# Kernel optimization log

Hardware: AMD Instinct MI355X
Metric: run time of the kernel (lower is better)

## Reference

```python
import jax, jax.numpy as jnp
import numpy as np
from jax import lax

# ---- config (mirrors cfg.* used by the module) ----
ANCHOR_RATIOS = (0.5, 1.0, 2.0)
ANCHOR_SCALES = (8.0, 16.0, 32.0)
FEATURE_STRIDE = 16
BASE_SIZE = 40  # generate_anchors(40, ...)
BN_EPS = 1e-5
LOG_CLAMP = 1e-30  # torch uses 1e-300, which underflows to 0 in fp32; use fp32-safe tiny


def generate_anchors(base_size=BASE_SIZE, ratios=ANCHOR_RATIOS, scales=ANCHOR_SCALES):
    """py-faster-rcnn style anchor generation, corner format (x1,y1,x2,y2). -> (A,4)"""
    w = h = float(base_size)
    cx = (base_size - 1) * 0.5
    cy = (base_size - 1) * 0.5
    size = w * h
    out = []
    for r in ratios:
        ws = np.round(np.sqrt(size / r))
        hs = np.round(ws * r)
        for s in scales:
            W, H = ws * s, hs * s
            out.append([cx - 0.5 * (W - 1), cy - 0.5 * (H - 1),
                        cx + 0.5 * (W - 1), cy + 0.5 * (H - 1)])
    return np.asarray(out, dtype=np.float32)  # (A,4)


def splash_anchors(fH, fW, n, base_anchors, stride):
    """Shift base anchors over the feature grid. -> (n, fH*fW*A, 4), row-major H,W then A."""
    sx = jnp.arange(fW, dtype=jnp.float32) * stride
    sy = jnp.arange(fH, dtype=jnp.float32) * stride
    SY, SX = jnp.meshgrid(sy, sx, indexing='ij')            # (fH,fW)
    shifts = jnp.stack([SX, SY, SX, SY], axis=-1).reshape(-1, 1, 4)  # (fH*fW,1,4)
    anc = (shifts + jnp.asarray(base_anchors)[None, :, :]).reshape(-1, 4)  # (fH*fW*A,4)
    return jnp.broadcast_to(anc[None], (n, anc.shape[0], 4))


def conv2d(x, w, b, pad):
    y = lax.conv_general_dilated(x, w, (1, 1), [(pad, pad), (pad, pad)],
                                 dimension_numbers=('NCHW', 'OIHW', 'NCHW'))
    return y + b[None, :, None, None]


def batchnorm_train(x, gamma, beta):
    # training-mode BN: per-channel batch stats over (N,H,W), biased variance
    m = jnp.mean(x, axis=(0, 2, 3), keepdims=True)
    v = jnp.mean(jnp.square(x - m), axis=(0, 2, 3), keepdims=True)
    xn = (x - m) * lax.rsqrt(v + BN_EPS)
    return xn * gamma[None, :, None, None] + beta[None, :, None, None]


def mish(x):
    return x * jnp.tanh(jax.nn.softplus(x))


def corner2center(b):
    w = b[..., 2] - b[..., 0]
    h = b[..., 3] - b[..., 1]
    cx = b[..., 0] + 0.5 * w
    cy = b[..., 1] + 0.5 * h
    return jnp.stack([cx, cy, w, h], axis=-1)


def setup_inputs() -> dict:
    key = jax.random.key(0)
    ks = jax.random.split(key, 7)
    C_IN, C_BASE, A = 256, 256, 9
    x = jax.random.normal(ks[0], (8, C_IN, 128, 128), dtype=jnp.float32)
    # kaiming-uniform-ish scaled weights
    def kaiming(k, shape):
        fan_in = shape[1] * shape[2] * shape[3]
        bound = float(np.sqrt(6.0 / fan_in))
        return jax.random.uniform(k, shape, jnp.float32, -bound, bound)
    return {
        "x": x,
        "W_base": kaiming(ks[1], (C_BASE, C_IN, 3, 3)),
        "b_base": jnp.zeros((C_BASE,), jnp.float32),
        "g_base": jnp.ones((C_BASE,), jnp.float32),
        "be_base": jnp.zeros((C_BASE,), jnp.float32),
        "W_cls": kaiming(ks[2], (2 * A, C_BASE, 1, 1)),
        "b_cls": jnp.zeros((2 * A,), jnp.float32),
        "g_cls": jnp.ones((2 * A,), jnp.float32),
        "be_cls": jnp.zeros((2 * A,), jnp.float32),
        "W_reg": kaiming(ks[3], (4 * A, C_BASE, 1, 1)),
        "b_reg": jnp.zeros((4 * A,), jnp.float32),
        "g_reg": jnp.ones((4 * A,), jnp.float32),
        "be_reg": jnp.zeros((4 * A,), jnp.float32),
        "img_size": 2048,
    }


def reference(x, W_base, b_base, g_base, be_base,
              W_cls, b_cls, g_cls, be_cls,
              W_reg, b_reg, g_reg, be_reg, img_size):
    n, c, fH, fW = x.shape
    A = 9
    # BASE_CONV: Conv3x3 -> Mish -> Dropout2d (identity here, deterministic) -> BN
    base = batchnorm_train(mish(conv2d(x, W_base, b_base, 1)), g_base, be_base)

    anchors = splash_anchors(fH, fW, n, generate_anchors(), FEATURE_STRIDE)  # (n,K,4) corners

    rpn_reg = batchnorm_train(conv2d(base, W_reg, b_reg, 0), g_reg, be_reg)
    rpn_reg = jnp.transpose(rpn_reg, (0, 2, 3, 1)).reshape(n, -1, 4)          # (n,K,4)

    rpn_score = batchnorm_train(conv2d(base, W_cls, b_cls, 0), g_cls, be_cls)
    rpn_score = jnp.transpose(rpn_score, (0, 2, 3, 1)).reshape(n, fH, fW, A, 2)
    fg_scores = jax.nn.softmax(rpn_score, axis=4)[..., 1].reshape(n, -1)      # (n,K)

    rpn_reg = rpn_reg + anchors                                               # decoded corners

    # proposal layer: clip proposals to the image, keep all (fixed-shape)
    lim = jnp.float32(img_size)
    rois = jnp.clip(rpn_reg, 0.0, lim)                                        # (n,K,4) corners
    rois = corner2center(rois)                                                # (cx,cy,w,h)

    anc_c = corner2center(anchors)
    tx = (rois[..., 0] - anc_c[..., 0]) / anc_c[..., 2]
    ty = (rois[..., 1] - anc_c[..., 1]) / anc_c[..., 3]
    tw = jnp.log(jnp.maximum(rois[..., 2] / anc_c[..., 2], LOG_CLAMP))
    th = jnp.log(jnp.maximum(rois[..., 3] / anc_c[..., 3], LOG_CLAMP))
    ts = jnp.stack([tx, ty, tw, th], axis=-1)
    return (fg_scores, ts, rois)
```

## Files before the change

### kernel.cpp

```cpp
#include <hip/hip_runtime.h>
#include <stdint.h>

typedef short bf16x8 __attribute__((ext_vector_type(8)));
typedef float f32x4 __attribute__((ext_vector_type(4)));

#define AS1 __attribute__((address_space(1)))
#define AS3 __attribute__((address_space(3)))

static __device__ __forceinline__ void gl16(const void* g, void* l) {
  __builtin_amdgcn_global_load_lds((const AS1 void*)g, (AS3 void*)l, 16, 0, 0);
}

static __device__ __forceinline__ unsigned short f2bf(float f) {
  unsigned u = __float_as_uint(f);
  u = u + 0x7fffu + ((u >> 16) & 1u);
  return (unsigned short)(u >> 16);
}
static __device__ __forceinline__ float bf2f(unsigned short h) {
  return __uint_as_float(((unsigned)h) << 16);
}
static __device__ __forceinline__ float mishf(float x) {
  float sp = fmaxf(x, 0.f) + log1pf(expf(-fabsf(x)));
  float e2 = expf(-2.f * sp);
  float th = (1.f - e2) / (1.f + e2);
  return x * th;
}

#define NIMG 8
#define HH 128
#define WW 128
#define HP 130
#define CIN 256
#define MPIX (NIMG * HH * WW)
#define KTOT 2304
#define FGCNT (MPIX * 9)
#define TSCNT (MPIX * 9 * 4)

__device__ __constant__ float AW[9] = {456.f, 912.f, 1824.f, 320.f, 640.f, 1280.f, 224.f, 448.f, 896.f};
__device__ __constant__ float AH[9] = {224.f, 448.f, 896.f, 320.f, 640.f, 1280.f, 448.f, 896.f, 1792.f};

__global__ __launch_bounds__(256) void k_wt(const float* __restrict__ Wb,
                                            unsigned short* __restrict__ Wt2) {
  int d = blockIdx.x * 256 + threadIdx.x;
  int c = d & 31, oc = (d >> 5) & 255, s = d >> 13;
  int icb = s / 9, khw = s % 9, kh = khw / 3, kw = khw % 3;
  int ic = icb * 32 + c;
  Wt2[d] = f2bf(Wb[((oc * 256 + ic) * 3 + kh) * 3 + kw]);
}

__global__ __launch_bounds__(256) void k_tr(const float* __restrict__ x,
                                            unsigned short* __restrict__ xt2) {
  __shared__ float tile[32][129];
  int b = blockIdx.x;
  int icb = b & 7, h = (b >> 3) & 127, n = b >> 10;
  int t = threadIdx.x;
  const float* src = x + (((size_t)(n * 256 + icb * 32) * 128 + h) * 128);
#pragma unroll
  for (int i = 0; i < 4; ++i) {
    int idx = t + 256 * i;
    int w4 = idx & 31, ic = idx >> 5;
    float4 v = *(const float4*)(src + (size_t)ic * 16384 + w4 * 4);
    tile[ic][w4 * 4 + 0] = v.x; tile[ic][w4 * 4 + 1] = v.y;
    tile[ic][w4 * 4 + 2] = v.z; tile[ic][w4 * 4 + 3] = v.w;
  }
  __syncthreads();
#pragma unroll
  for (int i = 0; i < 8; ++i) {
    int idx = t + 256 * i;
    int icp = idx & 15, w = idx >> 4;
    unsigned lo = f2bf(tile[icp * 2][w]);
    unsigned hi = f2bf(tile[icp * 2 + 1][w]);
    size_t pix = ((size_t)(icb * 8 + n) * HP + (h + 1)) * HP + (w + 1);
    *(unsigned*)(xt2 + pix * 32 + icp * 2) = lo | (hi << 16);
  }
}

__global__ __launch_bounds__(256) void k_bord(unsigned short* __restrict__ xt2) {
  int tid = blockIdx.x * 256 + threadIdx.x;
  int chunk = tid & 3, pix = tid >> 2;
  int nn = pix / 516, bp = pix % 516;
  int hp, wp;
  if (bp < 130) { hp = 0; wp = bp; }
  else if (bp < 260) { hp = 129; wp = bp - 130; }
  else { int r = bp - 260; hp = 1 + (r >> 1); wp = (r & 1) ? 129 : 0; }
  size_t off = (((size_t)nn * HP + hp) * HP + wp) * 32 + chunk * 8;
  uint4 z = {0u, 0u, 0u, 0u};
  *(uint4*)(xt2 + off) = z;
}

__global__ __launch_bounds__(256) void k_conv(const unsigned short* __restrict__ xt2,
                                              const unsigned short* __restrict__ Wt2,
                                              const float* __restrict__ b_base,
                                              unsigned short* __restrict__ yt2,
                                              float* __restrict__ statsA) {
  __shared__ __align__(16) char lds[49152];
  int t = threadIdx.x;
  int lane = t & 63, w4 = t >> 6;
  int wr = w4 >> 1, wc = w4 & 1;
  int row16 = lane & 15, kgl = lane >> 4;
  int pr = lane & 15, pq = lane >> 4;

  int bid = blockIdx.x;
  int swz = (bid & 7) * 256 + (bid >> 3);
  int pixb = swz >> 1, oh = swz & 1;
  int n = pixb >> 7, h0 = pixb & 127;
  size_t M0 = (size_t)pixb * 128;

  f32x4 acc[4][4];
#pragma unroll
  for (int m = 0; m < 4; ++m)
#pragma unroll
    for (int nf = 0; nf < 4; ++nf) { f32x4 z = {0.f, 0.f, 0.f, 0.f}; acc[m][nf] = z; }

  const unsigned short* aS0 =
      xt2 + ((size_t)(n * HP + h0) * HP + w4 * 32 + pr) * 32 + pq * 8;
  const unsigned short* aS1 = aS0 + 16 * 32;
  const unsigned short* bS0 = Wt2 + (size_t)(oh * 128 + w4 * 32 + pr) * 32 + pq * 8;
  const unsigned short* bS1 = bS0 + 16 * 32;

  const size_t planeStride = (size_t)8 * HP * HP * 32;
  int aoffA = wr * 4096 + kgl * 256 + row16 * 16;
  int aoffB = wc * 4096 + kgl * 256 + row16 * 16;

  auto STAGE = [&](int sv, int b_) {
    int icb_ = (sv * 57) >> 9;
    int khw = sv - icb_ * 9;
    int kh_ = (khw * 11) >> 5;
    int kw_ = khw - kh_ * 3;
    size_t offA = (size_t)icb_ * planeStride + ((size_t)kh_ * HP + kw_) * 32;
    size_t offB = (size_t)sv * 8192;
    char* buf = lds + b_ * 16384;
    gl16(aS0 + offA, buf + (2 * w4) * 1024);
    gl16(aS1 + offA, buf + (2 * w4 + 1) * 1024);
    gl16(bS0 + offB, buf + 8192 + (2 * w4) * 1024);
    gl16(bS1 + offB, buf + 8192 + (2 * w4 + 1) * 1024);
  };

  STAGE(0, 0);
  STAGE(1, 1);
  int cur = 0, nxt = 2;
  for (int s = 0; s < 72; ++s) {
    if (s < 71) { asm volatile("s_waitcnt vmcnt(4)" ::: "memory"); }
    else        { asm volatile("s_waitcnt vmcnt(0)" ::: "memory"); }
    __builtin_amdgcn_s_barrier();
    if (s < 70) STAGE(s + 2, nxt);
    const char* ab = lds + cur * 16384;
    const char* bb = ab + 8192;
    bf16x8 af[4], bfr[4];
#pragma unroll
    for (int m = 0; m < 4; ++m) af[m] = *(const bf16x8*)(ab + aoffA + m * 1024);
#pragma unroll
    for (int nf = 0; nf < 4; ++nf) bfr[nf] = *(const bf16x8*)(bb + aoffB + nf * 1024);
#pragma unroll
    for (int m = 0; m < 4; ++m)
#pragma unroll
      for (int nf = 0; nf < 4; ++nf)
        acc[m][nf] = __builtin_amdgcn_mfma_f32_16x16x32_bf16(af[m], bfr[nf], acc[m][nf], 0, 0, 0);
    cur = (cur == 2) ? 0 : cur + 1;
    nxt = (nxt == 2) ? 0 : nxt + 1;
  }

  float sums[4] = {0.f, 0.f, 0.f, 0.f}, sumq[4] = {0.f, 0.f, 0.f, 0.f};
#pragma unroll
  for (int nf = 0; nf < 4; ++nf) {
    int oc = oh * 128 + wc * 64 + nf * 16 + row16;
    float bias = b_base[oc];
    size_t obase = (size_t)(oc >> 5) * MPIX * 32 + (oc & 31);
#pragma unroll
    for (int m = 0; m < 4; ++m) {
#pragma unroll
      for (int j = 0; j < 4; ++j) {
        int p = wr * 64 + m * 16 + kgl * 4 + j;
        float y = mishf(acc[m][nf][j] + bias);
        yt2[obase + (M0 + p) * 32] = f2bf(y);
        sums[nf] += y; sumq[nf] += y * y;
      }
    }
  }
#pragma unroll
  for (int nf = 0; nf < 4; ++nf) {
    float s1 = sums[nf], s2 = sumq[nf];
    s1 += __shfl_xor(s1, 16); s2 += __shfl_xor(s2, 16);
    s1 += __shfl_xor(s1, 32); s2 += __shfl_xor(s2, 32);
    if (lane < 16) {
      int oc = oh * 128 + wc * 64 + nf * 16 + lane;
      atomicAdd(&statsA[oc], s1);
      atomicAdd(&statsA[256 + oc], s2);
    }
  }
}

__global__ __launch_bounds__(256) void k_fold(const float* __restrict__ statsA,
                                              const float* __restrict__ g_base,
                                              const float* __restrict__ be_base,
                                              const float* __restrict__ W_cls,
                                              const float* __restrict__ b_cls,
                                              const float* __restrict__ W_reg,
                                              const float* __restrict__ b_reg,
                                              unsigned short* __restrict__ W2t2,
                                              float* __restrict__ b2) {
  __shared__ float sS[256], sT[256];
  int t = threadIdx.x;
  {
    float cnt = (float)MPIX;
    float m = statsA[t] / cnt;
    float v = fmaxf(statsA[256 + t] / cnt - m * m, 0.f);
    float s = g_base[t] * rsqrtf(v + 1e-5f);
    sS[t] = s;
    sT[t] = be_base[t] - m * s;
  }
  __syncthreads();
  if (t < 64) {
    float bias = 0.f;
    if (t < 36) bias = b_reg[t];
    else if (t < 54) bias = b_cls[t - 36];
    float acc = 0.f;
    for (int ic = 0; ic < 256; ++ic) {
      float w = 0.f;
      if (t < 36) w = W_reg[t * 256 + ic];
      else if (t < 54) w = W_cls[(t - 36) * 256 + ic];
      acc += w * sT[ic];
      W2t2[((size_t)(ic >> 5) * 64 + t) * 32 + (ic & 31)] = f2bf(w * sS[ic]);
    }
    b2[t] = bias + acc;
  }
}

__global__ __launch_bounds__(256) void k_mm2(const unsigned short* __restrict__ yt2,
                                             const unsigned short* __restrict__ W2t2,
                                             const float* __restrict__ b2,
                                             unsigned short* __restrict__ zt,
                                             float* __restrict__ statsZ) {
  __shared__ __align__(16) char lds2[24576];
  int t = threadIdx.x, lane = t & 63, w4 = t >> 6;
  int row16 = lane & 15, kgl = lane >> 4;
  int pr = lane & 15, pq = lane >> 4;
  size_t pixbase = (size_t)blockIdx.x * 128;

  f32x4 acc[2][4];
#pragma unroll
  for (int m = 0; m < 2; ++m)
#pragma unroll
    for (int nn = 0; nn < 4; ++nn) { f32x4 z = {0.f, 0.f, 0.f, 0.f}; acc[m][nn] = z; }

  const unsigned short* aS0 = yt2 + (pixbase + w4 * 32 + pr) * 32 + pq * 8;
  const unsigned short* aS1 = aS0 + 16 * 32;
  const unsigned short* bS = W2t2 + (size_t)(w4 * 16 + pr) * 32 + pq * 8;

  int aoffA = w4 * 2048 + kgl * 256 + row16 * 16;
  int aoffB = kgl * 256 + row16 * 16;

  auto STG = [&](int s, int c_) {
    size_t ao = (size_t)s * MPIX * 32;
    size_t bo = (size_t)s * 2048;
    char* buf = lds2 + c_ * 12288;
    gl16(aS0 + ao, buf + (2 * w4) * 1024);
    gl16(aS1 + ao, buf + (2 * w4 + 1) * 1024);
    gl16(bS + bo, buf + 8192 + w4 * 1024);
  };

  STG(0, 0);
  int cur = 0;
  for (int s = 0; s < 8; ++s) {
    __syncthreads();
    if (s < 7) STG(s + 1, cur ^ 1);
    const char* ab = lds2 + cur * 12288;
    const char* bb = ab + 8192;
    bf16x8 af[2], bfr[4];
#pragma unroll
    for (int m = 0; m < 2; ++m) af[m] = *(const bf16x8*)(ab + aoffA + m * 1024);
#pragma unroll
    for (int nn = 0; nn < 4; ++nn) bfr[nn] = *(const bf16x8*)(bb + aoffB + nn * 1024);
#pragma unroll
    for (int m = 0; m < 2; ++m)
#pragma unroll
      for (int nn = 0; nn < 4; ++nn)
        acc[m][nn] = __builtin_amdgcn_mfma_f32_16x16x32_bf16(af[m], bfr[nn], acc[m][nn], 0, 0, 0);
    cur ^= 1;
  }

  float sums[4] = {0.f, 0.f, 0.f, 0.f}, sumq[4] = {0.f, 0.f, 0.f, 0.f};
#pragma unroll
  for (int nn = 0; nn < 4; ++nn) {
    int oc = nn * 16 + row16;
    float bias = b2[oc];
#pragma unroll
    for (int m = 0; m < 2; ++m) {
#pragma unroll
      for (int j = 0; j < 4; ++j) {
        int p = w4 * 32 + m * 16 + kgl * 4 + j;
        float v = acc[m][nn][j] + bias;
        zt[(pixbase + p) * 64 + oc] = f2bf(v);
        sums[nn] += v; sumq[nn] += v * v;
      }
    }
  }
#pragma unroll
  for (int nn = 0; nn < 4; ++nn) {
    float s1 = sums[nn], s2 = sumq[nn];
    s1 += __shfl_xor(s1, 16); s2 += __shfl_xor(s2, 16);
    s1 += __shfl_xor(s1, 32); s2 += __shfl_xor(s2, 32);
    if (lane < 16) {
      int oc = nn * 16 + lane;
      atomicAdd(&statsZ[oc], s1);
      atomicAdd(&statsZ[64 + oc], s2);
    }
  }
}

__global__ __launch_bounds__(64) void k_zstat(const float* __restrict__ statsZ,
                                              const float* __restrict__ g_cls,
                                              const float* __restrict__ be_cls,
                                              const float* __restrict__ g_reg,
                                              const float* __restrict__ be_reg,
                                              float* __restrict__ zsc,
                                              float* __restrict__ zsh) {
  int t = threadIdx.x;
  float g = 1.f, be = 0.f;
  if (t < 36) { g = g_reg[t]; be = be_reg[t]; }
  else if (t < 54) { g = g_cls[t - 36]; be = be_cls[t - 36]; }
  float cnt = (float)MPIX;
  float m = statsZ[t] / cnt;
  float v = fmaxf(statsZ[64 + t] / cnt - m * m, 0.f);
  float s = g * rsqrtf(v + 1e-5f);
  zsc[t] = s;
  zsh[t] = be - m * s;
}

__global__ __launch_bounds__(256) void k_dec(const unsigned short* __restrict__ zt,
                                             const float* __restrict__ zsc,
                                             const float* __restrict__ zsh,
                                             const int* __restrict__ imgsz,
                                             float* __restrict__ out) {
  int p = blockIdx.x * 256 + threadIdx.x;
  float lim = (float)imgsz[0];
  float zn[64];
  {
    const uint4* zp4 = (const uint4*)(zt + (size_t)p * 64);
#pragma unroll
    for (int i = 0; i < 8; ++i) {
      uint4 v = zp4[i];
      unsigned a0 = v.x, a1 = v.y, a2 = v.z, a3 = v.w;
      zn[i * 8 + 0] = bf2f((unsigned short)(a0 & 0xffff));
      zn[i * 8 + 1] = bf2f((unsigned short)(a0 >> 16));
      zn[i * 8 + 2] = bf2f((unsigned short)(a1 & 0xffff));
      zn[i * 8 + 3] = bf2f((unsigned short)(a1 >> 16));
      zn[i * 8 + 4] = bf2f((unsigned short)(a2 & 0xffff));
      zn[i * 8 + 5] = bf2f((unsigned short)(a2 >> 16));
      zn[i * 8 + 6] = bf2f((unsigned short)(a3 & 0xffff));
      zn[i * 8 + 7] = bf2f((unsigned short)(a3 >> 16));
    }
#pragma unroll
    for (int i = 0; i < 54; ++i) zn[i] = zn[i] * zsc[i] + zsh[i];
  }
  int rem = p & 16383, h = rem >> 7, w = rem & 127;
  float fx = 16.f * (float)w, fy = 16.f * (float)h;
  size_t kbase = (size_t)p * 9;
  float* fgout = out;
  float* tsout = out + FGCNT;
  float* roout = out + FGCNT + TSCNT;
#pragma unroll
  for (int a = 0; a < 9; ++a) {
    float x1 = 20.f - 0.5f * AW[a] + fx;
    float y1 = 20.f - 0.5f * AH[a] + fy;
    float x2 = 19.f + 0.5f * AW[a] + fx;
    float y2 = 19.f + 0.5f * AH[a] + fy;
    float cx1 = fminf(fmaxf(x1 + zn[4 * a + 0], 0.f), lim);
    float cy1 = fminf(fmaxf(y1 + zn[4 * a + 1], 0.f), lim);
    float cx2 = fminf(fmaxf(x2 + zn[4 * a + 2], 0.f), lim);
    float cy2 = fminf(fmaxf(y2 + zn[4 * a + 3], 0.f), lim);
    float bw = cx2 - cx1, bh = cy2 - cy1;
    float cx = cx1 + 0.5f * bw, cy = cy1 + 0.5f * bh;
    float aw = AW[a] - 1.f, ah = AH[a] - 1.f;
    float acx = 19.5f + fx, acy = 19.5f + fy;
    float tx = (cx - acx) / aw, ty = (cy - acy) / ah;
    float tw = logf(fmaxf(bw / aw, 1e-30f));
    float th = logf(fmaxf(bh / ah, 1e-30f));
    float s0 = zn[36 + 2 * a], s1 = zn[36 + 2 * a + 1];
    float fg = 1.f / (1.f + expf(s0 - s1));
    fgout[kbase + a] = fg;
    size_t o4 = (kbase + a) * 4;
    tsout[o4 + 0] = tx; tsout[o4 + 1] = ty; tsout[o4 + 2] = tw; tsout[o4 + 3] = th;
    roout[o4 + 0] = cx; roout[o4 + 1] = cy; roout[o4 + 2] = bw; roout[o4 + 3] = bh;
  }
}

extern "C" void kernel_launch(void* const* d_in, const int* in_sizes, int n_in,
                              void* d_out, int out_size, void* d_ws, size_t ws_size,
                              hipStream_t stream) {
  const float* x   = (const float*)d_in[0];
  const float* Wb  = (const float*)d_in[1];
  const float* bb  = (const float*)d_in[2];
  const float* gb  = (const float*)d_in[3];
  const float* beb = (const float*)d_in[4];
  const float* Wc  = (const float*)d_in[5];
  const float* bc  = (const float*)d_in[6];
  const float* gc  = (const float*)d_in[7];
  const float* bec = (const float*)d_in[8];
  const float* Wr  = (const float*)d_in[9];
  const float* br  = (const float*)d_in[10];
  const float* gr  = (const float*)d_in[11];
  const float* ber = (const float*)d_in[12];
  const int* imgsz = (const int*)d_in[13];

  char* ws = (char*)d_ws;
  const size_t OFF_XTP = 0;
  const size_t OFF_Y   = 69222400;
  const size_t OFF_Z   = 136331264;
  const size_t OFF_WT  = 153108480;
  const size_t OFF_W2  = 154288128;
  const size_t OFF_S   = 154320896;
  unsigned short* xt2  = (unsigned short*)(ws + OFF_XTP);
  unsigned short* yt2  = (unsigned short*)(ws + OFF_Y);
  unsigned short* zt   = (unsigned short*)(ws + OFF_Z);
  unsigned short* Wt2  = (unsigned short*)(ws + OFF_WT);
  unsigned short* W2t2 = (unsigned short*)(ws + OFF_W2);
  float* b2     = (float*)(ws + OFF_S);
  float* statsA = (float*)(ws + OFF_S + 256);
  float* statsZ = (float*)(ws + OFF_S + 2304);
  float* zsc    = (float*)(ws + OFF_S + 2816);
  float* zsh    = (float*)(ws + OFF_S + 3072);
  float* out = (float*)d_out;

  hipMemsetAsync(statsA, 0, (512 + 128) * sizeof(float), stream);
  k_wt  <<<2304, 256, 0, stream>>>(Wb, Wt2);
  k_tr  <<<8192, 256, 0, stream>>>(x, xt2);
  k_bord<<<516, 256, 0, stream>>>(xt2);
  k_conv<<<2048, 256, 0, stream>>>(xt2, Wt2, bb, yt2, statsA);
  k_fold<<<1, 256, 0, stream>>>(statsA, gb, beb, Wc, bc, Wr, br, W2t2, b2);
  k_mm2 <<<1024, 256, 0, stream>>>(yt2, W2t2, b2, zt, statsZ);
  k_zstat<<<1, 64, 0, stream>>>(statsZ, gc, bec, gr, ber, zsc, zsh);
  k_dec <<<512, 256, 0, stream>>>(zt, zsc, zsh, imgsz, out);
}
```

Measured before the change: 532.4 us.

## Split k_fold reduction across all threads and enlarge k_mm2 blocks to 512 threads

k_fold now uses all 256 threads. Each group of 64 threads handles a quarter of the input channels, writes the folded weights, and puts partial bias sums in shared memory that are then combined. Before, only 64 threads looped serially over 256 channels. k_mm2 now runs 512-thread blocks covering 256 pixels, with a larger double-buffered LDS tile in which only half the waves load the shared weight slice. This halves the grid and amortizes the weight staging over more pixels, at the cost of higher LDS use per block and possibly lower occupancy.

Result: faster. 502.0 us (-5.7%).

```diff
diff --git a/kernel.cpp b/kernel.cpp
--- a/kernel.cpp
+++ b/kernel.cpp
@@ -199,7 +199,7 @@
                                               const float* __restrict__ b_reg,
                                               unsigned short* __restrict__ W2t2,
                                               float* __restrict__ b2) {
-  __shared__ float sS[256], sT[256];
+  __shared__ float sS[256], sT[256], sP[4][64];
   int t = threadIdx.x;
   {
     float cnt = (float)MPIX;
@@ -210,32 +210,37 @@
     sT[t] = be_base[t] - m * s;
   }
   __syncthreads();
+  {
+    int oc = t & 63, part = t >> 6;
+    float accw = 0.f;
+    for (int ic = part * 64; ic < part * 64 + 64; ++ic) {
+      float w = 0.f;
+      if (oc < 36) w = W_reg[oc * 256 + ic];
+      else if (oc < 54) w = W_cls[(oc - 36) * 256 + ic];
+      accw += w * sT[ic];
+      W2t2[((size_t)(ic >> 5) * 64 + oc) * 32 + (ic & 31)] = f2bf(w * sS[ic]);
+    }
+    sP[part][oc] = accw;
+  }
+  __syncthreads();
   if (t < 64) {
     float bias = 0.f;
     if (t < 36) bias = b_reg[t];
     else if (t < 54) bias = b_cls[t - 36];
-    float acc = 0.f;
-    for (int ic = 0; ic < 256; ++ic) {
-      float w = 0.f;
-      if (t < 36) w = W_reg[t * 256 + ic];
-      else if (t < 54) w = W_cls[(t - 36) * 256 + ic];
-      acc += w * sT[ic];
-      W2t2[((size_t)(ic >> 5) * 64 + t) * 32 + (ic & 31)] = f2bf(w * sS[ic]);
-    }
-    b2[t] = bias + acc;
-  }
-}
-
-__global__ __launch_bounds__(256) void k_mm2(const unsigned short* __restrict__ yt2,
+    b2[t] = bias + sP[0][t] + sP[1][t] + sP[2][t] + sP[3][t];
+  }
+}
+
+__global__ __launch_bounds__(512) void k_mm2(const unsigned short* __restrict__ yt2,
                                              const unsigned short* __restrict__ W2t2,
                                              const float* __restrict__ b2,
                                              unsigned short* __restrict__ zt,
                                              float* __restrict__ statsZ) {
-  __shared__ __align__(16) char lds2[24576];
+  __shared__ __align__(16) char lds2[40960];
   int t = threadIdx.x, lane = t & 63, w4 = t >> 6;
   int row16 = lane & 15, kgl = lane >> 4;
   int pr = lane & 15, pq = lane >> 4;
-  size_t pixbase = (size_t)blockIdx.x * 128;
+  size_t pixbase = (size_t)blockIdx.x * 256;
 
   f32x4 acc[2][4];
 #pragma unroll
@@ -243,9 +248,9 @@
 #pragma unroll
     for (int nn = 0; nn < 4; ++nn) { f32x4 z = {0.f, 0.f, 0.f, 0.f}; acc[m][nn] = z; }
 
-  const unsigned short* aS0 = yt2 + (pixbase + w4 * 32 + pr) * 32 + pq * 8;
-  const unsigned short* aS1 = aS0 + 16 * 32;
-  const unsigned short* bS = W2t2 + (size_t)(w4 * 16 + pr) * 32 + pq * 8;
+  const unsigned short* aSrc0 = yt2 + (pixbase + w4 * 16 + pr) * 32 + pq * 8;
+  const unsigned short* aSrc1 = yt2 + (pixbase + 128 + w4 * 16 + pr) * 32 + pq * 8;
+  const unsigned short* bSrc  = W2t2 + (size_t)(w4 * 16 + pr) * 32 + pq * 8;
 
   int aoffA = w4 * 2048 + kgl * 256 + row16 * 16;
   int aoffB = kgl * 256 + row16 * 16;
@@ -253,10 +258,10 @@
   auto STG = [&](int s, int c_) {
     size_t ao = (size_t)s * MPIX * 32;
     size_t bo = (size_t)s * 2048;
-    char* buf = lds2 + c_ * 12288;
-    gl16(aS0 + ao, buf + (2 * w4) * 1024);
-    gl16(aS1 + ao, buf + (2 * w4 + 1) * 1024);
-    gl16(bS + bo, buf + 8192 + w4 * 1024);
+    char* buf = lds2 + c_ * 20480;
+    gl16(aSrc0 + ao, buf + w4 * 1024);
+    gl16(aSrc1 + ao, buf + (8 + w4) * 1024);
+    if (w4 < 4) gl16(bSrc + bo, buf + 16384 + w4 * 1024);
   };
 
   STG(0, 0);
@@ -264,8 +269,8 @@
   for (int s = 0; s < 8; ++s) {
     __syncthreads();
     if (s < 7) STG(s + 1, cur ^ 1);
-    const char* ab = lds2 + cur * 12288;
-    const char* bb = ab + 8192;
+    const char* ab = lds2 + cur * 20480;
+    const char* bb = ab + 16384;
     bf16x8 af[2], bfr[4];
 #pragma unroll
     for (int m = 0; m < 2; ++m) af[m] = *(const bf16x8*)(ab + aoffA + m * 1024);
@@ -428,7 +433,7 @@
   k_bord<<<516, 256, 0, stream>>>(xt2);
   k_conv<<<2048, 256, 0, stream>>>(xt2, Wt2, bb, yt2, statsA);
   k_fold<<<1, 256, 0, stream>>>(statsA, gb, beb, Wc, bc, Wr, br, W2t2, b2);
-  k_mm2 <<<1024, 256, 0, stream>>>(yt2, W2t2, b2, zt, statsZ);
+  k_mm2 <<<512, 512, 0, stream>>>(yt2, W2t2, b2, zt, statsZ);
   k_zstat<<<1, 64, 0, stream>>>(statsZ, gc, bec, gr, ber, zsc, zsh);
   k_dec <<<512, 256, 0, stream>>>(zt, zsc, zsh, imgsz, out);
 }
```
